# Optimization experiments

Hardware: AMD Instinct MI355X
Metric: run time of the kernel (lower is better)

Reference implementation:

```python
import jax, jax.numpy as jnp
import numpy as np

NEG = 1e9


def setup_inputs() -> dict:
    key = jax.random.key(0)
    k1, k2, k3 = jax.random.split(key, 3)
    B, Tq, Tv, D = 8, 2048, 2048, 512
    query = jax.random.normal(k1, (B, Tq, D), dtype=jnp.float32)
    value = jax.random.normal(k2, (B, Tv, D), dtype=jnp.float32)
    # length-style masks: every row has at least one valid position
    q_len = jax.random.randint(k3, (B,), Tq // 2, Tq + 1)
    v_len = jax.random.randint(jax.random.fold_in(k3, 1), (B,), Tv // 2, Tv + 1)
    q_mask = jnp.arange(Tq)[None, :] < q_len[:, None]
    v_mask = jnp.arange(Tv)[None, :] < v_len[:, None]
    return {"query": query, "value": value, "q_mask": q_mask, "v_mask": v_mask}


def reference(query, value, q_mask, v_mask):
    # key = value (2-input case); dot-product scores: [B, Tq, Tv]
    scores = jnp.einsum("bqd,bvd->bqv", query, value)
    Tq, Tv = scores.shape[-2], scores.shape[-1]
    # causal lower-triangular mask [1, Tq, Tv]
    causal = (jnp.arange(Tq)[:, None] >= jnp.arange(Tv)[None, :])[None]
    # merge value mask [B, 1, Tv] with causal mask
    scores_mask = jnp.logical_and(v_mask[:, None, :], causal)
    scores = scores - NEG * (~scores_mask).astype(scores.dtype)
    attn = jax.nn.softmax(scores, axis=-1)
    result = jnp.einsum("bqv,bvd->bqd", attn, value)
    # zero out masked query positions
    result = result * q_mask[:, :, None].astype(result.dtype)
    return result
```

## Files before the change

kernel.cpp:

```cpp
#include <hip/hip_runtime.h>
#include <hip/hip_bf16.h>
#include <cstdint>
#include <cstddef>


#define TQ   2048
#define TV   2048
#define DIM  512
#define NB   8
#define NROW (NB * TQ)
#define NSLOT 63

typedef _Float16 f16x8 __attribute__((ext_vector_type(8)));
typedef _Float16 f16x4 __attribute__((ext_vector_type(4)));
typedef float    f32x4 __attribute__((ext_vector_type(4)));
typedef int      i32x4 __attribute__((ext_vector_type(4)));

__device__ __forceinline__ int sched_ns(int g) { return (g + 11) / 11; }
__device__ __forceinline__ int sched_start(int g) {
    return (g < 11) ? g : ((g < 22) ? (2 * g - 11) : (3 * g - 33));
}

__device__ __forceinline__ int mask_fmt(const void* qm) {
    const unsigned* p = (const unsigned*)qm;
    unsigned w0 = p[0];
    if (w0 & 0xFF00u) return 0;
    unsigned w1 = p[1];
    if (w0 == 1u) return (w1 != 0u) ? 1 : 2;
    return 3;
}
__device__ __forceinline__ bool mask_bit(const void* m, int fmt, size_t i) {
    if (fmt == 0) return ((const unsigned char*)m)[i] != 0;
    if (fmt == 1) return ((const int*)m)[i] != 0;
    if (fmt == 2) return ((const unsigned*)m)[2 * i] != 0;
    return ((const float*)m)[i] != 0.0f;
}

__device__ __forceinline__ void gload_lds16(const void* g, void* l) {
    __builtin_amdgcn_global_load_lds(
        (const __attribute__((address_space(1))) unsigned int*)g,
        (__attribute__((address_space(3))) unsigned int*)l, 16, 0, 0);
}

__global__ void cvt_f16_kernel(const float* __restrict__ in, _Float16* __restrict__ out, int n8) {
    int i = blockIdx.x * blockDim.x + threadIdx.x;
    if (i >= n8) return;
    f32x4 x0 = *(const f32x4*)(in + (size_t)i * 8);
    f32x4 x1 = *(const f32x4*)(in + (size_t)i * 8 + 4);
    f16x8 o;
#pragma unroll
    for (int j = 0; j < 4; ++j) { o[j] = (_Float16)x0[j]; o[4 + j] = (_Float16)x1[j]; }
    *(f16x8*)(out + (size_t)i * 8) = o;
}

__global__ __launch_bounds__(256)
void prep_v_kernel(const float* __restrict__ vf, _Float16* __restrict__ wv,
                   _Float16* __restrict__ wvt) {
    __shared__ float sT[64][65];
    int z   = blockIdx.x;
    int b   = z & 7;
    int tv0 = ((z >> 3) & 31) * 64;
    int d0  = (z >> 8) * 64;
    int tid = threadIdx.x;
    int vl  = tid >> 4;
    int dq  = (tid & 15) * 4;
#pragma unroll
    for (int i = 0; i < 4; ++i) {
        int v = vl + i * 16;
        f32x4 x = *(const f32x4*)(vf + ((size_t)b * TV + tv0 + v) * DIM + d0 + dq);
        f16x4 h;
#pragma unroll
        for (int j = 0; j < 4; ++j) { h[j] = (_Float16)x[j]; sT[v][dq + j] = x[j]; }
        *(f16x4*)(wv + ((size_t)b * TV + tv0 + v) * DIM + d0 + dq) = h;
    }
    __syncthreads();
    int dl = tid >> 4;
    int vq = (tid & 15) * 4;
#pragma unroll
    for (int i = 0; i < 4; ++i) {
        int dloc = dl + i * 16;
        f16x4 h;
#pragma unroll
        for (int j = 0; j < 4; ++j) h[j] = (_Float16)sT[vq + j][dloc];
        *(f16x4*)(wvt + ((size_t)b * DIM + d0 + dloc) * TV + tv0 + vq) = h;
    }
}

__global__ __launch_bounds__(512)
__attribute__((amdgpu_waves_per_eu(2, 2)))
void attn_kernel(const _Float16* __restrict__ wq, const _Float16* __restrict__ wv,
                 const _Float16* __restrict__ wvt,
                 const void* __restrict__ qmask, const void* __restrict__ vmask,
                 _Float16* __restrict__ pacc, float* __restrict__ pml) {
    __shared__ __align__(16) _Float16 sV[2][32 * 512];
    __shared__ __align__(16) char     sVT[2][512 * 80];
    __shared__ unsigned sMW[64];

    const int tid  = threadIdx.x;
    const int lane = tid & 63;
    const int w    = tid >> 6;
    const int q16  = lane & 15;
    const int grp  = lane >> 4;

    const int bid  = blockIdx.x;
    const int b    = bid & 7;
    const int slot = (NSLOT - 1) - (bid >> 3);

    int g = 0, s = 0;
#pragma unroll
    for (int j = 0; j < 32; ++j) {
        int st = sched_start(j);
        if (slot >= st && slot < st + sched_ns(j)) { g = j; s = slot - st; }
    }
    const int NSg = sched_ns(g);

    const int pairId = w >> 1;
    const int dhalf  = w & 1;
    const int qtile  = 4 * g + pairId;
    const int qrow   = qtile * 16 + q16;
    const size_t qrowG = (size_t)b * TQ + qrow;
    const int bound = qtile >> 1;

    const int fmt = mask_fmt(qmask);

    unsigned long long qbal = __ballot(mask_bit(qmask, fmt, (size_t)b * TQ + g * 64 + lane));
    const bool waveActive = ((qbal >> (16 * pairId)) & 0xFFFFull) != 0ull;
    int bmaxb = -1;
#pragma unroll
    for (int ti = 0; ti < 4; ++ti)
        if ((qbal >> (16 * ti)) & 0xFFFFull) bmaxb = max(bmaxb, (4 * g + ti) >> 1);

    if (w == 0) {
#pragma unroll
        for (int c = 0; c < 32; ++c) {
            unsigned long long bal = __ballot(mask_bit(vmask, fmt, (size_t)b * TV + c * 64 + lane));
            if (lane == 0) {
                sMW[2 * c]     = (unsigned)(bal & 0xFFFFFFFFull);
                sMW[2 * c + 1] = (unsigned)(bal >> 32);
            }
        }
    }

    f16x8 qreg[16];
    if (waveActive) {
#pragma unroll
        for (int kc = 0; kc < 16; ++kc)
            qreg[kc] = *(const f16x8*)(wq + qrowG * DIM + kc * 32 + grp * 8);
    }

    auto stage = [&](int buf, int tt) {
#pragma unroll
        for (int k = 0; k < 4; ++k) {
            int vr = w * 4 + k;
            const _Float16* src = wv + ((size_t)b * TV + tt * 32 + vr) * DIM
                                     + ((lane ^ ((vr & 7) << 2)) << 3);
            gload_lds16(src, (char*)&sV[buf][0] + vr * 1024);
        }
#pragma unroll
        for (int k = 0; k < 5; ++k) {
            int slot2 = k * 64 + lane;
            int dloc  = slot2 / 5;
            int c     = slot2 - dloc * 5;
            int cs    = (c >= 4) ? 0 : c;
            const _Float16* src = wvt + ((size_t)b * DIM + w * 64 + dloc) * TV + tt * 32 + cs * 8;
            gload_lds16(src, &sVT[buf][0] + w * 5120 + k * 1024);
        }
    };

    f32x4 acc[16];
#pragma unroll
    for (int c = 0; c < 16; ++c) acc[c] = (f32x4){0.f, 0.f, 0.f, 0.f};
    float m_run = -3.0e38f, l_run = 0.0f;

    const int sw = (q16 & 7) << 2;

    if (bmaxb >= s) {
        stage(0, s);
        int t1 = s + NSg; if (t1 > bmaxb) t1 = bmaxb;
        stage(1, t1);
        asm volatile("s_waitcnt vmcnt(9) lgkmcnt(0)" ::: "memory");
        __builtin_amdgcn_s_barrier();

        int cur = 0;
        for (int t = s; t <= bmaxb; t += NSg) {
            const int vb = t * 32;
            const unsigned mw = sMW[t];
            if (mw == 0u) break;
            const bool act = waveActive && (t <= bound);
            const _Float16* sVc  = &sV[cur][0];
            const char*     sVTc = &sVT[cur][0];

            f32x4 s0a = (f32x4){0.f,0.f,0.f,0.f}, s0b = s0a, s1a = s0a, s1b = s0a;
            if (act) {
                __builtin_amdgcn_s_setprio(1);
#pragma unroll
                for (int kc = 0; kc < 16; kc += 2) {
                    int c0 = ((kc * 4 + grp) ^ sw) << 4;
                    int c1 = (((kc + 1) * 4 + grp) ^ sw) << 4;
                    f16x8 a00 = *(const f16x8*)((const char*)sVc + q16 * 1024 + c0);
                    s0a = __builtin_amdgcn_mfma_f32_16x16x32_f16(a00, qreg[kc], s0a, 0, 0, 0);
                    f16x8 a10 = *(const f16x8*)((const char*)sVc + (16 + q16) * 1024 + c0);
                    s1a = __builtin_amdgcn_mfma_f32_16x16x32_f16(a10, qreg[kc], s1a, 0, 0, 0);
                    f16x8 a01 = *(const f16x8*)((const char*)sVc + q16 * 1024 + c1);
                    s0b = __builtin_amdgcn_mfma_f32_16x16x32_f16(a01, qreg[kc + 1], s0b, 0, 0, 0);
                    f16x8 a11 = *(const f16x8*)((const char*)sVc + (16 + q16) * 1024 + c1);
                    s1b = __builtin_amdgcn_mfma_f32_16x16x32_f16(a11, qreg[kc + 1], s1b, 0, 0, 0);
                }
                __builtin_amdgcn_s_setprio(0);

                f32x4 s0 = s0a + s0b, s1 = s1a + s1b;
                float p[8];
                float tm = -3.0e38f;
#pragma unroll
                for (int i = 0; i < 8; ++i) {
                    int vloc = ((i < 4) ? 0 : 16) + grp * 4 + (i & 3);
                    float x = (i < 4) ? s0[i] : s1[i - 4];
                    bool valid = ((vb + vloc) <= qrow) && ((mw >> vloc) & 1u);
                    x = valid ? x : (x - 1e9f);
                    p[i] = x;
                    tm = fmaxf(tm, x);
                }
                tm = fmaxf(tm, __shfl_xor(tm, 16, 64));
                tm = fmaxf(tm, __shfl_xor(tm, 32, 64));
                if (!__all(tm <= m_run + 8.0f)) {
                    float mn = fmaxf(m_run, tm);
                    float rr = __expf(m_run - mn);
                    l_run *= rr;
#pragma unroll
                    for (int c = 0; c < 16; ++c) acc[c] *= rr;
                    m_run = mn;
                }
                float ps = 0.0f;
#pragma unroll
                for (int i = 0; i < 8; ++i) { p[i] = __expf(p[i] - m_run); ps += p[i]; }
                ps += __shfl_xor(ps, 16, 64);
                ps += __shfl_xor(ps, 32, 64);
                l_run += ps;

                int pk0 = __builtin_bit_cast(int, __builtin_amdgcn_cvt_pkrtz(p[0], p[1]));
                int pk1 = __builtin_bit_cast(int, __builtin_amdgcn_cvt_pkrtz(p[2], p[3]));
                int pk2 = __builtin_bit_cast(int, __builtin_amdgcn_cvt_pkrtz(p[4], p[5]));
                int pk3 = __builtin_bit_cast(int, __builtin_amdgcn_cvt_pkrtz(p[6], p[7]));
                int lo = q16 + ((grp & 1) << 5);
                int hi = lo + 16;
                int a0 = __shfl(pk0, lo, 64);
                int a1 = __shfl(pk1, lo, 64);
                int a2 = __shfl(pk0, hi, 64);
                int a3 = __shfl(pk1, hi, 64);
                int c0s = __shfl(pk2, lo, 64);
                int c1s = __shfl(pk3, lo, 64);
                int c2s = __shfl(pk2, hi, 64);
                int c3s = __shfl(pk3, hi, 64);
                bool hb = (grp & 2) != 0;
                i32x4 f;
                f[0] = hb ? c0s : a0;
                f[1] = hb ? c1s : a1;
                f[2] = hb ? c2s : a2;
                f[3] = hb ? c3s : a3;
                f16x8 pf = __builtin_bit_cast(f16x8, f);

                __builtin_amdgcn_s_setprio(1);
#pragma unroll
                for (int c = 0; c < 16; ++c) {
                    int d = dhalf * 256 + c * 16 + q16;
                    f16x8 a = *(const f16x8*)(sVTc + d * 80 + (grp << 4));
                    acc[c] = __builtin_amdgcn_mfma_f32_16x16x32_f16(a, pf, acc[c], 0, 0, 0);
                }
                __builtin_amdgcn_s_setprio(0);
            }
            __builtin_amdgcn_s_barrier();
            int t2 = t + 2 * NSg; if (t2 > bmaxb) t2 = bmaxb;
            stage(cur, t2);
            asm volatile("s_waitcnt vmcnt(9)" ::: "memory");
            __builtin_amdgcn_s_barrier();
            cur ^= 1;
        }
    }
    asm volatile("s_waitcnt vmcnt(0) lgkmcnt(0)" ::: "memory");

    float inv = (l_run > 0.f) ? (1.0f / l_run) : 0.0f;
    int rowInB = pairId * 16 + q16;
    _Float16* pb = pacc + (((size_t)(b * NSLOT + slot) * 64) + rowInB) * DIM;
#pragma unroll
    for (int c = 0; c < 16; ++c) {
        f16x4 hh;
#pragma unroll
        for (int j = 0; j < 4; ++j) hh[j] = (_Float16)(acc[c][j] * inv);
        *(f16x4*)(pb + dhalf * 256 + c * 16 + grp * 4) = hh;
    }
    if (dhalf == 0 && grp == 0) {
        size_t mi = (((size_t)(b * NSLOT + slot) * 64) + rowInB) * 2;
        pml[mi]     = m_run;
        pml[mi + 1] = l_run;
    }
}

__global__ __launch_bounds__(256)
void combine_kernel(const _Float16* __restrict__ pacc, const float* __restrict__ pml,
                    const void* __restrict__ qmask, float* __restrict__ out) {
    int gid = blockIdx.x * 256 + threadIdx.x;
    int row = gid >> 7;
    int c   = (gid & 127) * 4;
    if (row >= NROW) return;
    int b      = row >> 11;
    int local  = row & 2047;
    int g      = local >> 6;
    int rowInG = local & 63;
    int ns     = sched_ns(g);
    int st     = sched_start(g);

    float m = -3.0e38f;
    for (int s2 = 0; s2 < ns; ++s2) {
        size_t idx = ((size_t)(b * NSLOT + st + s2) * 64) + rowInG;
        float l2 = pml[idx * 2 + 1];
        if (l2 > 0.f) m = fmaxf(m, pml[idx * 2]);
    }
    float L = 0.f;
    f32x4 o = (f32x4){0.f, 0.f, 0.f, 0.f};
    for (int s2 = 0; s2 < ns; ++s2) {
        size_t idx = ((size_t)(b * NSLOT + st + s2) * 64) + rowInG;
        float l2 = pml[idx * 2 + 1];
        if (l2 > 0.f) {
            float wgt = __expf(pml[idx * 2] - m) * l2;
            L += wgt;
            f16x4 hh = *(const f16x4*)(pacc + idx * DIM + c);
#pragma unroll
            for (int j = 0; j < 4; ++j) o[j] += wgt * (float)hh[j];
        }
    }
    int fmt = mask_fmt(qmask);
    bool qb = mask_bit(qmask, fmt, (size_t)row);
    float invL = (L > 0.f && qb) ? (1.0f / L) : 0.f;
    o *= invL;
    *(f32x4*)(out + (size_t)row * DIM + c) = o;
}

extern "C" void kernel_launch(void* const* d_in, const int* in_sizes, int n_in,
                              void* d_out, int out_size, void* d_ws, size_t ws_size,
                              hipStream_t stream) {
    const float* q = (const float*)d_in[0];
    const float* v = (const float*)d_in[1];
    const void* qm = d_in[2];
    const void* vm = d_in[3];
    float* out = (float*)d_out;

    const size_t nElem = (size_t)NB * TQ * DIM;
    const size_t wqB   = nElem * sizeof(_Float16);
    const size_t wvB   = wqB, wvtB = wqB;
    const size_t paccB = (size_t)NB * NSLOT * 64 * DIM * sizeof(_Float16);
    const size_t pmlB  = (size_t)NB * NSLOT * 64 * 2 * sizeof(float);

    if (ws_size < wqB + wvB + wvtB + paccB + pmlB) {
        (void)hipMemsetAsync(d_out, 0, (size_t)out_size * sizeof(float), stream);
        return;
    }
    _Float16* wq   = (_Float16*)d_ws;
    _Float16* wv   = (_Float16*)((char*)d_ws + wqB);
    _Float16* wvt  = (_Float16*)((char*)d_ws + wqB + wvB);
    _Float16* pacc = (_Float16*)((char*)d_ws + wqB + wvB + wvtB);
    float*    pml  = (float*)((char*)d_ws + wqB + wvB + wvtB + paccB);

    int n8 = (int)(nElem / 8);
    cvt_f16_kernel<<<dim3(n8 / 256), dim3(256), 0, stream>>>(q, wq, n8);
    prep_v_kernel<<<dim3(2048), dim3(256), 0, stream>>>(v, wv, wvt);
    attn_kernel<<<dim3(NB * NSLOT), dim3(512), 0, stream>>>(wq, wv, wvt, qm, vm, pacc, pml);
    combine_kernel<<<dim3(NROW * 128 / 256), dim3(256), 0, stream>>>(pacc, pml, qm, out);
}
```

Baseline: 177.8 us.

## Single-buffer LDS staging with split sV/sVT loads to raise occupancy

Replaces the double-buffered V and V-transpose LDS tiles with single buffers and splits staging so the next V tile loads after QK^T and the next V^T tile loads after PV, using extra barriers and vmcnt waits. The waves-per-EU hint is raised from 2 to 4 so two blocks can share a CU. This aims to hide latency through occupancy rather than prefetch depth, but it halves the register budget per thread while the kernel holds large accumulator and query register arrays, which risks spills, and it adds more barriers per tile.

```diff
diff --git a/kernel.cpp b/kernel.cpp
--- a/kernel.cpp
+++ b/kernel.cpp
@@ -87,13 +87,13 @@
 }
 
 __global__ __launch_bounds__(512)
-__attribute__((amdgpu_waves_per_eu(2, 2)))
+__attribute__((amdgpu_waves_per_eu(4, 4)))
 void attn_kernel(const _Float16* __restrict__ wq, const _Float16* __restrict__ wv,
                  const _Float16* __restrict__ wvt,
                  const void* __restrict__ qmask, const void* __restrict__ vmask,
                  _Float16* __restrict__ pacc, float* __restrict__ pml) {
-    __shared__ __align__(16) _Float16 sV[2][32 * 512];
-    __shared__ __align__(16) char     sVT[2][512 * 80];
+    __shared__ __align__(16) _Float16 sV[32 * 512];
+    __shared__ __align__(16) char     sVT[512 * 80];
     __shared__ unsigned sMW[64];
 
     const int tid  = threadIdx.x;
@@ -148,14 +148,16 @@
             qreg[kc] = *(const f16x8*)(wq + qrowG * DIM + kc * 32 + grp * 8);
     }
 
-    auto stage = [&](int buf, int tt) {
+    auto stage_sV = [&](int tt) {
 #pragma unroll
         for (int k = 0; k < 4; ++k) {
             int vr = w * 4 + k;
             const _Float16* src = wv + ((size_t)b * TV + tt * 32 + vr) * DIM
                                      + ((lane ^ ((vr & 7) << 2)) << 3);
-            gload_lds16(src, (char*)&sV[buf][0] + vr * 1024);
-        }
+            gload_lds16(src, (char*)sV + vr * 1024);
+        }
+    };
+    auto stage_sVT = [&](int tt) {
 #pragma unroll
         for (int k = 0; k < 5; ++k) {
             int slot2 = k * 64 + lane;
@@ -163,7 +165,7 @@
             int c     = slot2 - dloc * 5;
             int cs    = (c >= 4) ? 0 : c;
             const _Float16* src = wvt + ((size_t)b * DIM + w * 64 + dloc) * TV + tt * 32 + cs * 8;
-            gload_lds16(src, &sVT[buf][0] + w * 5120 + k * 1024);
+            gload_lds16(src, sVT + w * 5120 + k * 1024);
         }
     };
 
@@ -175,20 +177,17 @@
     const int sw = (q16 & 7) << 2;
 
     if (bmaxb >= s) {
-        stage(0, s);
-        int t1 = s + NSg; if (t1 > bmaxb) t1 = bmaxb;
-        stage(1, t1);
-        asm volatile("s_waitcnt vmcnt(9) lgkmcnt(0)" ::: "memory");
+        stage_sV(s);
+        stage_sVT(s);
+        asm volatile("s_waitcnt vmcnt(0) lgkmcnt(0)" ::: "memory");
         __builtin_amdgcn_s_barrier();
 
-        int cur = 0;
         for (int t = s; t <= bmaxb; t += NSg) {
             const int vb = t * 32;
             const unsigned mw = sMW[t];
             if (mw == 0u) break;
             const bool act = waveActive && (t <= bound);
-            const _Float16* sVc  = &sV[cur][0];
-            const char*     sVTc = &sVT[cur][0];
+            int tn = t + NSg; if (tn > bmaxb) tn = bmaxb;
 
             f32x4 s0a = (f32x4){0.f,0.f,0.f,0.f}, s0b = s0a, s1a = s0a, s1b = s0a;
             if (act) {
@@ -197,17 +196,22 @@
                 for (int kc = 0; kc < 16; kc += 2) {
                     int c0 = ((kc * 4 + grp) ^ sw) << 4;
                     int c1 = (((kc + 1) * 4 + grp) ^ sw) << 4;
-                    f16x8 a00 = *(const f16x8*)((const char*)sVc + q16 * 1024 + c0);
+                    f16x8 a00 = *(const f16x8*)((const char*)sV + q16 * 1024 + c0);
                     s0a = __builtin_amdgcn_mfma_f32_16x16x32_f16(a00, qreg[kc], s0a, 0, 0, 0);
-                    f16x8 a10 = *(const f16x8*)((const char*)sVc + (16 + q16) * 1024 + c0);
+                    f16x8 a10 = *(const f16x8*)((const char*)sV + (16 + q16) * 1024 + c0);
                     s1a = __builtin_amdgcn_mfma_f32_16x16x32_f16(a10, qreg[kc], s1a, 0, 0, 0);
-                    f16x8 a01 = *(const f16x8*)((const char*)sVc + q16 * 1024 + c1);
+                    f16x8 a01 = *(const f16x8*)((const char*)sV + q16 * 1024 + c1);
                     s0b = __builtin_amdgcn_mfma_f32_16x16x32_f16(a01, qreg[kc + 1], s0b, 0, 0, 0);
-                    f16x8 a11 = *(const f16x8*)((const char*)sVc + (16 + q16) * 1024 + c1);
+                    f16x8 a11 = *(const f16x8*)((const char*)sV + (16 + q16) * 1024 + c1);
                     s1b = __builtin_amdgcn_mfma_f32_16x16x32_f16(a11, qreg[kc + 1], s1b, 0, 0, 0);
                 }
                 __builtin_amdgcn_s_setprio(0);
-
+            }
+            __builtin_amdgcn_s_barrier();
+            stage_sV(tn);
+
+            f16x8 pf;
+            if (act) {
                 f32x4 s0 = s0a + s0b, s1 = s1a + s1b;
                 float p[8];
                 float tm = -3.0e38f;
@@ -257,23 +261,25 @@
                 f[1] = hb ? c1s : a1;
                 f[2] = hb ? c2s : a2;
                 f[3] = hb ? c3s : a3;
-                f16x8 pf = __builtin_bit_cast(f16x8, f);
-
+                pf = __builtin_bit_cast(f16x8, f);
+            }
+            asm volatile("s_waitcnt vmcnt(4)" ::: "memory");
+            __builtin_amdgcn_s_barrier();
+
+            if (act) {
                 __builtin_amdgcn_s_setprio(1);
 #pragma unroll
                 for (int c = 0; c < 16; ++c) {
                     int d = dhalf * 256 + c * 16 + q16;
-                    f16x8 a = *(const f16x8*)(sVTc + d * 80 + (grp << 4));
+                    f16x8 a = *(const f16x8*)(sVT + d * 80 + (grp << 4));
                     acc[c] = __builtin_amdgcn_mfma_f32_16x16x32_f16(a, pf, acc[c], 0, 0, 0);
                 }
                 __builtin_amdgcn_s_setprio(0);
             }
             __builtin_amdgcn_s_barrier();
-            int t2 = t + 2 * NSg; if (t2 > bmaxb) t2 = bmaxb;
-            stage(cur, t2);
-            asm volatile("s_waitcnt vmcnt(9)" ::: "memory");
+            stage_sVT(tn);
+            asm volatile("s_waitcnt vmcnt(5)" ::: "memory");
             __builtin_amdgcn_s_barrier();
-            cur ^= 1;
         }
     }
     asm volatile("s_waitcnt vmcnt(0) lgkmcnt(0)" ::: "memory");
```

Result: slower. 681.2 us (+283.1%).
